# Kernel optimization log

Measured on AMD Instinct MI355X. Metric: run time of the kernel, lower is better.

Reference implementation:

```python
import jax, jax.numpy as jnp
import numpy as np

N = 50000   # nodes
E = 800000  # edges
IN, H, OUT = 64, 512, 128


def _lin_init(key, out_dim, in_dim):
    kw, kb = jax.random.split(key)
    bound = 1.0 / np.sqrt(in_dim)
    W = jax.random.uniform(kw, (out_dim, in_dim), jnp.float32, -bound, bound)
    b = jax.random.uniform(kb, (out_dim,), jnp.float32, -bound, bound)
    return W, b


def setup_inputs() -> dict:
    key = jax.random.key(0)
    ks = jax.random.split(key, 10)
    x = jax.random.normal(ks[0], (N, IN), jnp.float32)
    edge_index = jax.random.randint(ks[1], (2, E), 0, N, jnp.int64)
    W_s1, b_s1 = _lin_init(ks[2], H, IN)
    W_s2, b_s2 = _lin_init(ks[3], H, H)
    W_s3, b_s3 = _lin_init(ks[4], H, H)
    W_s4, b_s4 = _lin_init(ks[5], H, H)
    W_m1, b_m1 = _lin_init(ks[6], OUT, H)
    W_m2, b_m2 = _lin_init(ks[7], OUT, OUT)
    W_l1, b_l1 = _lin_init(ks[8], OUT, H)
    W_l2, b_l2 = _lin_init(ks[9], OUT, OUT)
    return {"x": x, "edge_index": edge_index,
            "W_s1": W_s1, "b_s1": b_s1, "W_s2": W_s2, "b_s2": b_s2,
            "W_s3": W_s3, "b_s3": b_s3, "W_s4": W_s4, "b_s4": b_s4,
            "W_m1": W_m1, "b_m1": b_m1, "W_m2": W_m2, "b_m2": b_m2,
            "W_l1": W_l1, "b_l1": b_l1, "W_l2": W_l2, "b_l2": b_l2}


def _aggregate(h, src, dst):
    # GINConv with default eps=0: (1+eps)*x + sum_{j in N(i)} x_j
    return h + jax.ops.segment_sum(h[src], dst, num_segments=N)


def reference(x, edge_index,
              W_s1, b_s1, W_s2, b_s2, W_s3, b_s3, W_s4, b_s4,
              W_m1, b_m1, W_m2, b_m2, W_l1, b_l1, W_l2, b_l2):
    src, dst = edge_index[0], edge_index[1]
    lrelu = lambda v: jax.nn.leaky_relu(v, 0.1)

    def mlp_shared(h):
        h = lrelu(h @ W_s1.T + b_s1)
        h = lrelu(h @ W_s2.T + b_s2)
        h = lrelu(h @ W_s3.T + b_s3)
        return h @ W_s4.T + b_s4

    def mlp_mu(h):
        return jax.nn.relu(h @ W_m1.T + b_m1) @ W_m2.T + b_m2

    def mlp_logvar(h):
        return jax.nn.relu(h @ W_l1.T + b_l1) @ W_l2.T + b_l2

    h = jax.nn.relu(mlp_shared(_aggregate(x, src, dst)))
    mu = mlp_mu(_aggregate(h, src, dst))
    logvar = mlp_logvar(_aggregate(h, src, dst))
    return (mu, logvar)
```

## Files before the change

### kernel.cpp

```cpp
#include <hip/hip_runtime.h>
#include <hip/hip_bf16.h>
#include <stdint.h>

#define N_NODES 50000
#define N_PAD   50048
#define E_EDGES 800000
#define MT      391

typedef __bf16 bf16x8 __attribute__((ext_vector_type(8)));
typedef __bf16 bf16x4 __attribute__((ext_vector_type(4)));
typedef float  f32x4  __attribute__((ext_vector_type(4)));

#define SCAN_B 1024
__global__ void scan_block(const int* __restrict__ cnt, int* __restrict__ ptr,
                           int* __restrict__ bsum, int n) {
    __shared__ int buf[SCAN_B];
    int i = blockIdx.x * SCAN_B + threadIdx.x;
    int v = (i < n) ? cnt[i] : 0;
    buf[threadIdx.x] = v;
    __syncthreads();
    #pragma unroll
    for (int off = 1; off < SCAN_B; off <<= 1) {
        int t = (threadIdx.x >= (unsigned)off) ? buf[threadIdx.x - off] : 0;
        __syncthreads();
        buf[threadIdx.x] += t;
        __syncthreads();
    }
    if (i < n) ptr[i] = buf[threadIdx.x] - v;
    if (threadIdx.x == SCAN_B - 1) bsum[blockIdx.x] = buf[SCAN_B - 1];
}

__global__ void scan_bsums(const int* __restrict__ bsum, int* __restrict__ boff,
                           int nb, int* __restrict__ total_out) {
    __shared__ int buf[SCAN_B];
    int v = ((int)threadIdx.x < nb) ? bsum[threadIdx.x] : 0;
    buf[threadIdx.x] = v;
    __syncthreads();
    #pragma unroll
    for (int off = 1; off < SCAN_B; off <<= 1) {
        int t = (threadIdx.x >= (unsigned)off) ? buf[threadIdx.x - off] : 0;
        __syncthreads();
        buf[threadIdx.x] += t;
        __syncthreads();
    }
    if ((int)threadIdx.x < nb) boff[threadIdx.x] = buf[threadIdx.x] - v;
    if (threadIdx.x == SCAN_B - 1) *total_out = buf[SCAN_B - 1];
}

__global__ void scan_add(int* __restrict__ ptr, const int* __restrict__ boff, int n) {
    int i = blockIdx.x * SCAN_B + threadIdx.x;
    if (i < n) ptr[i] += boff[blockIdx.x];
}

__global__ void fill_csr(const int* __restrict__ ei, const int* __restrict__ ptr,
                         int* __restrict__ cursor, int* __restrict__ col) {
    int e = blockIdx.x * blockDim.x + threadIdx.x;
    if (e < E_EDGES) {
        int dst = ei[E_EDGES + e];
        int pos = ptr[dst] + atomicAdd(&cursor[dst], 1);
        col[pos] = ei[e];
    }
}

#define XN      3200000
#define WTOT    983040
__global__ void cvt_count(const float* __restrict__ x,
                          const float* __restrict__ Ws1, const float* __restrict__ Ws2,
                          const float* __restrict__ Ws3, const float* __restrict__ Ws4,
                          const float* __restrict__ Wm1, const float* __restrict__ Wl1,
                          const float* __restrict__ Wm2, const float* __restrict__ Wl2,
                          const int* __restrict__ ei,
                          __bf16* __restrict__ xb, __bf16* __restrict__ wbuf,
                          int* __restrict__ cnt) {
    int i = blockIdx.x * blockDim.x + threadIdx.x;
    if (i < XN) { xb[i] = (__bf16)x[i]; return; }
    int j = i - XN;
    if (j < WTOT) {
        const float* s; int o;
        if      (j <  32768) { s = Ws1; o = j; }
        else if (j < 294912) { s = Ws2; o = j -  32768; }
        else if (j < 557056) { s = Ws3; o = j - 294912; }
        else if (j < 819200) { s = Ws4; o = j - 557056; }
        else if (j < 884736) { s = Wm1; o = j - 819200; }
        else if (j < 950272) { s = Wl1; o = j - 884736; }
        else if (j < 966656) { s = Wm2; o = j - 950272; }
        else                 { s = Wl2; o = j - 966656; }
        wbuf[j] = (__bf16)s[o];
        return;
    }
    int e = j - WTOT;
    if (e < E_EDGES) atomicAdd(&cnt[ei[E_EDGES + e]], 1);
}

__global__ __launch_bounds__(256) void agg0_gather(
    const __bf16* __restrict__ xb, const int* __restrict__ ptr,
    const int* __restrict__ col, __bf16* __restrict__ out) {
    int node = blockIdx.x * 4 + (threadIdx.x >> 6);
    int lane = threadIdx.x & 63;
    int g    = lane >> 3;
    int f0   = (lane & 7) << 3;
    if (node >= N_PAD) return;
    long o = (long)node * 64 + f0;
    if (node >= N_NODES) {
        if (g == 0) {
            bf16x8 z;
            #pragma unroll
            for (int i = 0; i < 8; ++i) z[i] = (__bf16)0.0f;
            *(bf16x8*)&out[o] = z;
        }
        return;
    }
    float a[8];
    #pragma unroll
    for (int i = 0; i < 8; ++i) a[i] = 0.0f;
    if (g == 0) {
        bf16x8 s = *(const bf16x8*)&xb[o];
        #pragma unroll
        for (int i = 0; i < 8; ++i) a[i] = (float)s[i];
    }
    int e0 = ptr[node], e1 = ptr[node + 1];
    int e = e0;
    for (; e + 16 <= e1; e += 16) {
        int c0 = col[e + g];
        int c1 = col[e + 8 + g];
        bf16x8 v0 = *(const bf16x8*)&xb[(c0 << 6) + f0];
        bf16x8 v1 = *(const bf16x8*)&xb[(c1 << 6) + f0];
        #pragma unroll
        for (int i = 0; i < 8; ++i) a[i] += (float)v0[i] + (float)v1[i];
    }
    int rem = e1 - e;
    if (rem > 0) {
        int u0 = (g < rem) ? g : 0;        float m0 = (g < rem) ? 1.0f : 0.0f;
        int i1 = g + 8;
        int u1 = (i1 < rem) ? i1 : 0;      float m1 = (i1 < rem) ? 1.0f : 0.0f;
        int c0 = col[e + u0];
        int c1 = col[e + u1];
        bf16x8 v0 = *(const bf16x8*)&xb[(c0 << 6) + f0];
        bf16x8 v1 = *(const bf16x8*)&xb[(c1 << 6) + f0];
        #pragma unroll
        for (int i = 0; i < 8; ++i) a[i] += m0 * (float)v0[i] + m1 * (float)v1[i];
    }
    #pragma unroll
    for (int i = 0; i < 8; ++i) {
        a[i] += __shfl_xor(a[i], 8, 64);
        a[i] += __shfl_xor(a[i], 16, 64);
        a[i] += __shfl_xor(a[i], 32, 64);
    }
    if (g == 0) {
        bf16x8 r;
        #pragma unroll
        for (int i = 0; i < 8; ++i) r[i] = (__bf16)a[i];
        *(bf16x8*)&out[o] = r;
    }
}

__global__ __launch_bounds__(256) void aggt_gather(
    const __bf16* __restrict__ t, const int* __restrict__ ptr,
    const int* __restrict__ col, const float* __restrict__ b_m1,
    const float* __restrict__ b_l1, __bf16* __restrict__ p) {
    int node = blockIdx.x * 8 + (threadIdx.x >> 5);
    if (node >= N_NODES) return;
    int hl = threadIdx.x & 31;
    int f0 = hl << 3;
    float a[8];
    {
        bf16x8 s = *(const bf16x8*)&t[((long)node << 8) + f0];
        #pragma unroll
        for (int i = 0; i < 8; ++i) a[i] = (float)s[i];
    }
    int e0 = ptr[node], e1 = ptr[node + 1];
    int e = e0;
    for (; e + 8 <= e1; e += 8) {
        int c[8];
        #pragma unroll
        for (int u = 0; u < 8; ++u) c[u] = col[e + u];
        bf16x8 v[8];
        #pragma unroll
        for (int u = 0; u < 8; ++u) v[u] = *(const bf16x8*)&t[((long)c[u] << 8) + f0];
        #pragma unroll
        for (int u = 0; u < 8; ++u)
            #pragma unroll
            for (int i = 0; i < 8; ++i) a[i] += (float)v[u][i];
    }
    int rem = e1 - e;
    if (rem > 0) {
        #pragma unroll
        for (int u = 0; u < 7; ++u) {
            int   uu = (u < rem) ? u : 0;
            float m  = (u < rem) ? 1.0f : 0.0f;
            int   cc = col[e + uu];
            bf16x8 v = *(const bf16x8*)&t[((long)cc << 8) + f0];
            #pragma unroll
            for (int i = 0; i < 8; ++i) a[i] += m * (float)v[i];
        }
    }
    const float* bp = (f0 < 128) ? (b_m1 + f0) : (b_l1 + (f0 - 128));
    f32x4 b0 = *(const f32x4*)bp;
    f32x4 b1 = *(const f32x4*)(bp + 4);
    bf16x8 r;
    #pragma unroll
    for (int i = 0; i < 4; ++i) r[i]     = (__bf16)fmaxf(a[i]     + b0[i], 0.0f);
    #pragma unroll
    for (int i = 0; i < 4; ++i) r[4 + i] = (__bf16)fmaxf(a[4 + i] + b1[i], 0.0f);
    *(bf16x8*)&p[((long)node << 8) + f0] = r;
}

__device__ __forceinline__ void gl_lds16(const __bf16* g, __bf16* l) {
    __builtin_amdgcn_global_load_lds(
        (const __attribute__((address_space(1))) uint32_t*)g,
        (__attribute__((address_space(3))) uint32_t*)l, 16, 0, 0);
}

#define P_WAITN(n) asm volatile("s_waitcnt vmcnt(" #n ")" ::: "memory")
#define P_WAIT0    asm volatile("s_waitcnt vmcnt(0)" ::: "memory")
#define P_LGKM0    asm volatile("s_waitcnt lgkmcnt(0)" ::: "memory")
#define P_BAR      __builtin_amdgcn_s_barrier()
#define P_SGB      __builtin_amdgcn_sched_barrier(0)
#define SLOTE      2048

__device__ __forceinline__ void stage_w64(const __bf16* __restrict__ W, int Kdim,
                                          int k0, int wn,
                                          __bf16* __restrict__ slot, int lane) {
    int r16 = lane >> 2, sl = lane & 3;
    #pragma unroll
    for (int i = 0; i < 4; ++i) {
        int rl = i * 16 + r16;
        int kt = sl ^ ((rl >> 1) & 3);
        gl_lds16(W + (long)(wn + rl) * Kdim + k0 + kt * 8, slot + i * 512);
    }
}

__device__ __forceinline__ void stage_wp32(const __bf16* __restrict__ W, int k0,
                                           int wnp, __bf16* __restrict__ slot,
                                           int lane) {
    int r8 = lane >> 3, sl = lane & 7;
    #pragma unroll
    for (int i = 0; i < 4; ++i) {
        int rl = i * 8 + r8;
        int kt = sl ^ (rl & 7);
        gl_lds16(W + (long)(wnp + rl) * 512 + k0 + kt * 8, slot + i * 512);
    }
}

__device__ __forceinline__ void chunk_mfma4L(const __bf16* __restrict__ sAct,
    const __bf16* __restrict__ buf, int c, int rA, int q,
    f32x4 (&acc)[4][4]) {
    const int g   = c * 4 + q;
    const int sla = ((g & 56) | ((g & 7) ^ (rA & 7))) << 3;
    bf16x8 af[4], bfr[4];
    #pragma unroll
    for (int mi = 0; mi < 4; ++mi)
        af[mi] = *(const bf16x8*)&sAct[(mi * 16 + rA) * 512 + sla];
    #pragma unroll
    for (int ni = 0; ni < 4; ++ni) {
        int wrl = ni * 16 + rA;
        bfr[ni] = *(const bf16x8*)&buf[wrl * 32 + ((q ^ ((wrl >> 1) & 3)) << 3)];
    }
    #pragma unroll
    for (int mi = 0; mi < 4; ++mi)
        #pragma unroll
        for (int ni = 0; ni < 4; ++ni)
            acc[mi][ni] = __builtin_amdgcn_mfma_f32_16x16x32_bf16(
                af[mi], bfr[ni], acc[mi][ni], 0, 0, 0);
}

__device__ __forceinline__ void chunk_mfma_a0L(const __bf16* __restrict__ act0,
    const __bf16* __restrict__ buf, int c, int rA, int q,
    f32x4 (&acc)[4][4]) {
    const int g   = c * 4 + q;
    const int sla = (g ^ (rA & 7)) << 3;
    bf16x8 af[4], bfr[4];
    #pragma unroll
    for (int mi = 0; mi < 4; ++mi)
        af[mi] = *(const bf16x8*)&act0[(mi * 16 + rA) * 64 + sla];
    #pragma unroll
    for (int ni = 0; ni < 4; ++ni) {
        int wrl = ni * 16 + rA;
        bfr[ni] = *(const bf16x8*)&buf[wrl * 32 + ((q ^ ((wrl >> 1) & 3)) << 3)];
    }
    #pragma unroll
    for (int mi = 0; mi < 4; ++mi)
        #pragma unroll
        for (int ni = 0; ni < 4; ++ni)
            acc[mi][ni] = __builtin_amdgcn_mfma_f32_16x16x32_bf16(
                af[mi], bfr[ni], acc[mi][ni], 0, 0, 0);
}

__device__ __forceinline__ void chunk_mfma_projL(const __bf16* __restrict__ sAct,
    const __bf16* __restrict__ buf, int c, int rA, int q,
    f32x4 (&accp)[4][2]) {
    #pragma unroll
    for (int s = 0; s < 2; ++s) {
        const int g   = c * 8 + s * 4 + q;
        const int sla = ((g & 56) | ((g & 7) ^ (rA & 7))) << 3;
        bf16x8 af[4], bfr[2];
        #pragma unroll
        for (int mi = 0; mi < 4; ++mi)
            af[mi] = *(const bf16x8*)&sAct[(mi * 16 + rA) * 512 + sla];
        #pragma unroll
        for (int ni = 0; ni < 2; ++ni) {
            int wrl = ni * 16 + rA;
            int gB  = s * 4 + q;
            bfr[ni] = *(const bf16x8*)&buf[wrl * 64 + ((gB ^ (wrl & 7)) << 3)];
        }
        #pragma unroll
        for (int mi = 0; mi < 4; ++mi)
            #pragma unroll
            for (int ni = 0; ni < 2; ++ni)
                accp[mi][ni] = __builtin_amdgcn_mfma_f32_16x16x32_bf16(
                    af[mi], bfr[ni], accp[mi][ni], 0, 0, 0);
    }
}

template <int ACTn>
__device__ __forceinline__ void writeback_act(__bf16* __restrict__ sAct,
    f32x4 (&acc)[4][4], const float* __restrict__ bv,
    int wn, int ccol, int crow) {
    #pragma unroll
    for (int mi = 0; mi < 4; ++mi)
        #pragma unroll
        for (int ni = 0; ni < 4; ++ni) {
            int cc = wn + ni * 16 + ccol;
            int g  = cc >> 3;
            #pragma unroll
            for (int p = 0; p < 4; ++p) {
                int rr = mi * 16 + crow + p;
                float v = acc[mi][ni][p] + bv[ni];
                if (ACTn == 1) v = (v > 0.0f) ? v : 0.1f * v;
                else           v = fmaxf(v, 0.0f);
                int sl = (g & 56) | ((g & 7) ^ (rr & 7));
                sAct[rr * 512 + sl * 8 + (cc & 7)] = (__bf16)v;
            }
        }
}

template <int ACTn, bool NPROJ>
__device__ __forceinline__ void layer512_wv(
    __bf16* __restrict__ sAct, __bf16* __restrict__ sA, __bf16* __restrict__ sB,
    const __bf16* __restrict__ W, const __bf16* __restrict__ Wn,
    const float* __restrict__ bv,
    int wn, int wnp, int rA, int q, int ccol, int crow, int lane) {
    f32x4 acc[4][4];
    #pragma unroll
    for (int i = 0; i < 4; ++i)
        #pragma unroll
        for (int j = 0; j < 4; ++j) acc[i][j] = (f32x4)0.0f;
    #pragma unroll
    for (int c = 0; c < 16; ++c) {
        P_WAITN(4);
        __bf16* cur = (c & 1) ? sB : sA;
        chunk_mfma4L(sAct, cur, c, rA, q, acc);
        P_SGB;
        if (c <= 13)      stage_w64(W, 512, (c + 2) * 32, wn, cur, lane);
        else if (!NPROJ)  stage_w64(Wn, 512, (c - 14) * 32, wn, cur, lane);
        else              stage_wp32(Wn, (c - 14) * 64, wnp, cur, lane);
    }
    P_BAR;
    writeback_act<ACTn>(sAct, acc, bv, wn, ccol, crow);
    P_LGKM0; P_BAR;
}

__global__ __launch_bounds__(512) void mlp_fused(
    const __bf16* __restrict__ a0,
    const __bf16* __restrict__ w1, const float* __restrict__ b1,
    const __bf16* __restrict__ w2, const float* __restrict__ b2,
    const __bf16* __restrict__ w3, const float* __restrict__ b3,
    const __bf16* __restrict__ w4, const float* __restrict__ b4,
    const __bf16* __restrict__ wp,
    __bf16* __restrict__ tg)
{
    __shared__ __bf16 lds[69632];
    __bf16* act0  = lds;
    __bf16* sAct  = lds + 4096;
    __bf16* slots = lds + 36864;

    const int tid  = threadIdx.x;
    const int wid  = tid >> 6;
    const int lane = tid & 63;
    const long blockRow = (long)blockIdx.x * 64;

    const int rA   = lane & 15;
    const int q    = lane >> 4;
    const int ccol = lane & 15;
    const int crow = (lane >> 4) << 2;
    const int wn   = wid << 6;
    const int wnp  = wid << 5;

    __bf16* sA = slots + (wid * 2) * SLOTE;
    __bf16* sB = sA + SLOTE;

    {
        int srow = lane >> 3;
        int skg  = (lane & 7) ^ srow;
        gl_lds16(a0 + (blockRow + wid * 8 + srow) * 64 + skg * 8, act0 + wid * 512);
    }
    stage_w64(w1, 64, 0,  wn, sA, lane);
    stage_w64(w1, 64, 32, wn, sB, lane);
    float bv1[4], bv2[4], bv3[4], bv4[4];
    #pragma unroll
    for (int ni = 0; ni < 4; ++ni) {
        int idx = wn + ni * 16 + ccol;
        bv1[ni] = b1[idx]; bv2[ni] = b2[idx]; bv3[ni] = b3[idx]; bv4[ni] = b4[idx];
    }

    asm volatile("s_waitcnt vmcnt(0) lgkmcnt(0)" ::: "memory");
    P_BAR;

    {
        f32x4 acc[4][4];
        #pragma unroll
        for (int i = 0; i < 4; ++i)
            #pragma unroll
            for (int j = 0; j < 4; ++j) acc[i][j] = (f32x4)0.0f;
        chunk_mfma_a0L(act0, sA, 0, rA, q, acc);
        P_SGB;
        stage_w64(w2, 512, 0, wn, sA, lane);
        P_WAITN(4);
        chunk_mfma_a0L(act0, sB, 1, rA, q, acc);
        P_SGB;
        stage_w64(w2, 512, 32, wn, sB, lane);
        P_BAR;
        writeback_act<1>(sAct, acc, bv1, wn, ccol, crow);
        P_LGKM0; P_BAR;
    }

    layer512_wv<1, false>(sAct, sA, sB, w2, w3, bv2, wn, wnp, rA, q, ccol, crow, lane);
    layer512_wv<1, false>(sAct, sA, sB, w3, w4, bv3, wn, wnp, rA, q, ccol, crow, lane);
    layer512_wv<2, true >(sAct, sA, sB, w4, wp, bv4, wn, wnp, rA, q, ccol, crow, lane);

    {
        f32x4 accp[4][2];
        #pragma unroll
        for (int i = 0; i < 4; ++i)
            #pragma unroll
            for (int j = 0; j < 2; ++j) accp[i][j] = (f32x4)0.0f;
        #pragma unroll
        for (int c = 0; c < 8; ++c) {
            if (c == 7) { P_WAIT0; } else { P_WAITN(4); }
            __bf16* cur = (c & 1) ? sB : sA;
            chunk_mfma_projL(sAct, cur, c, rA, q, accp);
            P_SGB;
            if (c <= 5) stage_wp32(wp, (c + 2) * 64, wnp, cur, lane);
        }
        P_BAR;
        __bf16* s0 = slots;
        #pragma unroll
        for (int mi = 0; mi < 4; ++mi)
            #pragma unroll
            for (int ni = 0; ni < 2; ++ni)
                #pragma unroll
                for (int p = 0; p < 4; ++p)
                    s0[(mi * 16 + crow + p) * 256 + wnp + ni * 16 + ccol] =
                        (__bf16)accp[mi][ni][p];
        __syncthreads();
        int rr = tid >> 3;
        int c0 = (tid & 7) << 5;
        const bf16x8* s = (const bf16x8*)&s0[rr * 256 + c0];
        __bf16* d = tg + (blockRow + rr) * 256 + c0;
        #pragma unroll
        for (int i = 0; i < 4; ++i) *(bf16x8*)(d + i * 8) = s[i];
    }
}

template <int NCOL>
__device__ __forceinline__ void swizzle_xy(int bid, int& x, int& y) {
    int grp  = bid / (8 * NCOL);
    int rem  = bid - grp * (8 * NCOL);
    int base = grp * 8;
    int width = MT - base; if (width > 8) width = 8;
    x = base + rem % width;
    y = rem / width;
}

template <int ACT, bool BIAS, bool OUT_BF16, bool MCHK>
__device__ __forceinline__ void gemm_core(
    const __bf16* __restrict__ A, int lda, const __bf16* __restrict__ W,
    const float* __restrict__ bias, void* __restrict__ Cout, int ldc,
    int K, long Mstore, long blockRow, int blockCol,
    __bf16* __restrict__ smem) {
    __bf16* As = smem;
    __bf16* Ws = smem + 8192;
    const int tid  = threadIdx.x;
    const int wid  = tid >> 6;
    const int lane = tid & 63;
    const int wm = (wid >> 1) << 6;
    const int wn = (wid & 1) << 6;

    f32x4 acc[4][4];
    #pragma unroll
    for (int i = 0; i < 4; ++i)
        #pragma unroll
        for (int j = 0; j < 4; ++j) acc[i][j] = (f32x4)0.0f;

    const int srow = lane >> 3;
    const int skg  = (lane & 7) ^ srow;
    const __bf16* gA[4]; const __bf16* gW[4];
    __bf16 *lA[4], *lW[4];
    #pragma unroll
    for (int i = 0; i < 4; ++i) {
        int c = wid * 4 + i;
        gA[i] = A + (blockRow + c * 8 + srow) * (long)lda + skg * 8;
        gW[i] = W + ((long)blockCol + c * 8 + srow) * (long)K + skg * 8;
        lA[i] = As + c * 512;
        lW[i] = Ws + c * 512;
    }

    const int rA = lane & 15;
    const int q  = lane >> 4;
    const int r7 = rA & 7;

    for (int k0 = 0; k0 < K; k0 += 64) {
        #pragma unroll
        for (int i = 0; i < 4; ++i) gl_lds16(gA[i] + k0, lA[i]);
        #pragma unroll
        for (int i = 0; i < 4; ++i) gl_lds16(gW[i] + k0, lW[i]);
        __syncthreads();

        #pragma unroll
        for (int s = 0; s < 2; ++s) {
            const int slot = ((s * 4 + q) ^ r7) * 8;
            bf16x8 af[4], bf[4];
            #pragma unroll
            for (int mi = 0; mi < 4; ++mi)
                af[mi] = *(const bf16x8*)&As[(wm + mi * 16 + rA) * 64 + slot];
            #pragma unroll
            for (int ni = 0; ni < 4; ++ni)
                bf[ni] = *(const bf16x8*)&Ws[(wn + ni * 16 + rA) * 64 + slot];
            #pragma unroll
            for (int mi = 0; mi < 4; ++mi)
                #pragma unroll
                for (int ni = 0; ni < 4; ++ni)
                    acc[mi][ni] = __builtin_amdgcn_mfma_f32_16x16x32_bf16(
                        af[mi], bf[ni], acc[mi][ni], 0, 0, 0);
        }
        __syncthreads();
    }

    const int ccol = lane & 15;
    const int crow = (lane >> 4) << 2;
    if (OUT_BF16 && !MCHK) {
        #pragma unroll
        for (int mi = 0; mi < 4; ++mi) {
            #pragma unroll
            for (int ni = 0; ni < 4; ++ni) {
                int gc = wn + ni * 16 + ccol;
                float bv = BIAS ? bias[blockCol + gc] : 0.0f;
                #pragma unroll
                for (int r = 0; r < 4; ++r) {
                    float v = acc[mi][ni][r] + bv;
                    if (ACT == 1) v = (v > 0.0f) ? v : 0.1f * v;
                    else if (ACT == 2) v = fmaxf(v, 0.0f);
                    smem[(wm + mi * 16 + crow + r) * 128 + gc] = (__bf16)v;
                }
            }
        }
        __syncthreads();
        #pragma unroll
        for (int i = 0; i < 8; ++i) {
            int o   = (i * 256 + tid) * 8;
            int row = o >> 7;
            int co  = o & 127;
            *(bf16x8*)((__bf16*)Cout + (blockRow + row) * (long)ldc + blockCol + co) =
                *(const bf16x8*)&smem[o];
        }
    } else if (!OUT_BF16) {
        float* fsmem = (float*)smem;
        #pragma unroll
        for (int half = 0; half < 2; ++half) {
            __syncthreads();
            if ((wm >> 6) == half) {
                #pragma unroll
                for (int mi = 0; mi < 4; ++mi) {
                    #pragma unroll
                    for (int ni = 0; ni < 4; ++ni) {
                        int gc = wn + ni * 16 + ccol;
                        float bv = BIAS ? bias[blockCol + gc] : 0.0f;
                        #pragma unroll
                        for (int r = 0; r < 4; ++r) {
                            float v = acc[mi][ni][r] + bv;
                            if (ACT == 1) v = (v > 0.0f) ? v : 0.1f * v;
                            else if (ACT == 2) v = fmaxf(v, 0.0f);
                            fsmem[(mi * 16 + crow + r) * 128 + gc] = v;
                        }
                    }
                }
            }
            __syncthreads();
            #pragma unroll
            for (int i = 0; i < 8; ++i) {
                int o   = i * 256 + tid;
                int row = o >> 5;
                int co  = (o & 31) * 4;
                long gr = blockRow + half * 64 + row;
                if (!MCHK || gr < Mstore)
                    *(f32x4*)((float*)Cout + gr * (long)ldc + blockCol + co) =
                        *(const f32x4*)&fsmem[o * 4];
            }
        }
    } else {
        #pragma unroll
        for (int mi = 0; mi < 4; ++mi) {
            #pragma unroll
            for (int ni = 0; ni < 4; ++ni) {
                long gr0 = blockRow + wm + mi * 16 + crow;
                int  gc  = blockCol + wn + ni * 16 + ccol;
                float bv = BIAS ? bias[gc] : 0.0f;
                #pragma unroll
                for (int r = 0; r < 4; ++r) {
                    long gr = gr0 + r;
                    if (!MCHK || gr < Mstore) {
                        float v = acc[mi][ni][r] + bv;
                        if (ACT == 1) v = (v > 0.0f) ? v : 0.1f * v;
                        else if (ACT == 2) v = fmaxf(v, 0.0f);
                        ((__bf16*)Cout)[gr * ldc + gc] = (__bf16)v;
                    }
                }
            }
        }
    }
}

__global__ __launch_bounds__(256) void gemm_heads(
    const __bf16* __restrict__ p, const __bf16* __restrict__ wm2,
    const float* __restrict__ b_m2, float* __restrict__ mu,
    const __bf16* __restrict__ wl2, const float* __restrict__ b_l2,
    float* __restrict__ lv) {
    __shared__ __bf16 smem[128 * 128];
    int x, hd;
    swizzle_xy<2>(blockIdx.x, x, hd);
    if (hd == 0)
        gemm_core<0, true, false, true>(p, 256, wm2, b_m2, mu, 128, 128, N_NODES,
                                        (long)x * 128, 0, smem);
    else
        gemm_core<0, true, false, true>(p + 128, 256, wl2, b_l2, lv, 128, 128, N_NODES,
                                        (long)x * 128, 0, smem);
}

extern "C" void kernel_launch(void* const* d_in, const int* in_sizes, int n_in,
                              void* d_out, int out_size, void* d_ws, size_t ws_size,
                              hipStream_t stream) {
    const float* x    = (const float*)d_in[0];
    const int*   ei   = (const int*)d_in[1];
    const float* W_s1 = (const float*)d_in[2];
    const float* b_s1 = (const float*)d_in[3];
    const float* W_s2 = (const float*)d_in[4];
    const float* b_s2 = (const float*)d_in[5];
    const float* W_s3 = (const float*)d_in[6];
    const float* b_s3 = (const float*)d_in[7];
    const float* W_s4 = (const float*)d_in[8];
    const float* b_s4 = (const float*)d_in[9];
    const float* W_m1 = (const float*)d_in[10];
    const float* b_m1 = (const float*)d_in[11];
    const float* W_m2 = (const float*)d_in[12];
    const float* b_m2 = (const float*)d_in[13];
    const float* W_l1 = (const float*)d_in[14];
    const float* b_l1 = (const float*)d_in[15];
    const float* W_l2 = (const float*)d_in[16];
    const float* b_l2 = (const float*)d_in[17];

    char* ws = (char*)d_ws;
    size_t off = 0;
    auto carve = [&](size_t bytes) -> void* {
        void* p = ws + off;
        off = (off + bytes + 255) & ~(size_t)255;
        return p;
    };
    int* ptr  = (int*)carve((size_t)(N_NODES + 1) * 4);
    int* col  = (int*)carve((size_t)E_EDGES * 4);
    int* bsum = (int*)carve(SCAN_B * 4);
    int* boff = (int*)carve(SCAN_B * 4);
    __bf16* wbuf = (__bf16*)carve((size_t)WTOT * 2);
    __bf16* w1  = wbuf;
    __bf16* w2  = wbuf +  32768;
    __bf16* w3  = wbuf + 294912;
    __bf16* w4  = wbuf + 557056;
    __bf16* wml = wbuf + 819200;
    __bf16* wm2 = wbuf + 950272;
    __bf16* wl2 = wbuf + 966656;
    __bf16* xb    = (__bf16*)carve((size_t)XN * 2);
    __bf16* agg0b = (__bf16*)carve((size_t)N_PAD * 64 * 2);
    __bf16* B1    = (__bf16*)carve((size_t)N_PAD * 512 * 2);
    __bf16* B2    = (__bf16*)carve((size_t)N_PAD * 512 * 2);

    int* cnt = (int*)B1;
    int* cur = (int*)B2;

    (void)hipMemsetAsync(cnt, 0, (size_t)N_NODES * 4, stream);
    (void)hipMemsetAsync(cur, 0, (size_t)N_NODES * 4, stream);

    cvt_count<<<(XN + WTOT + E_EDGES + 255) / 256, 256, 0, stream>>>(
        x, W_s1, W_s2, W_s3, W_s4, W_m1, W_l1, W_m2, W_l2, ei, xb, wbuf, cnt);

    const int NB = (N_NODES + SCAN_B - 1) / SCAN_B;
    scan_block<<<NB, SCAN_B, 0, stream>>>(cnt, ptr, bsum, N_NODES);
    scan_bsums<<<1, SCAN_B, 0, stream>>>(bsum, boff, NB, &ptr[N_NODES]);
    scan_add<<<NB, SCAN_B, 0, stream>>>(ptr, boff, N_NODES);
    fill_csr<<<E_EDGES / 256, 256, 0, stream>>>(ei, ptr, cur, col);

    agg0_gather<<<N_PAD / 4, 256, 0, stream>>>(xb, ptr, col, agg0b);

    __bf16* t = B1;
    mlp_fused<<<N_PAD / 64, 512, 0, stream>>>(agg0b, w1, b_s1, w2, b_s2,
                                              w3, b_s3, w4, b_s4, wml, t);

    __bf16* p = B2;
    aggt_gather<<<(N_NODES + 7) / 8, 256, 0, stream>>>(t, ptr, col, b_m1, b_l1, p);

    float* mu = (float*)d_out;
    float* lv = mu + (size_t)N_NODES * 128;
    gemm_heads<<<MT * 2, 256, 0, stream>>>(p, wm2, b_m2, mu, wl2, b_l2, lv);
}
```

Baseline: 426.0 us.

## Fuse second-layer neighbor gather into the mu/logvar head GEMM kernel

Replaces the separate aggregation kernel (which wrote the aggregated, bias+ReLU hidden tensor p to global memory) and the head GEMM kernel with a single kernel. Each block gathers neighbor sums for its 128 nodes and one head's 128 columns directly into swizzled LDS, then runs the 128x128x128 MFMA GEMM and writes fp32 outputs. This removes the p write/read round-trip and one launch. In exchange each block does its gather with only 256 threads in 8 sequential passes, which may reduce memory-level parallelism, and it uses 64KB of LDS per block, which limits occupancy.

```diff
diff --git a/kernel.cpp b/kernel.cpp
--- a/kernel.cpp
+++ b/kernel.cpp
@@ -154,61 +154,20 @@
     }
 }
 
-__global__ __launch_bounds__(256) void aggt_gather(
-    const __bf16* __restrict__ t, const int* __restrict__ ptr,
-    const int* __restrict__ col, const float* __restrict__ b_m1,
-    const float* __restrict__ b_l1, __bf16* __restrict__ p) {
-    int node = blockIdx.x * 8 + (threadIdx.x >> 5);
-    if (node >= N_NODES) return;
-    int hl = threadIdx.x & 31;
-    int f0 = hl << 3;
-    float a[8];
-    {
-        bf16x8 s = *(const bf16x8*)&t[((long)node << 8) + f0];
-        #pragma unroll
-        for (int i = 0; i < 8; ++i) a[i] = (float)s[i];
-    }
-    int e0 = ptr[node], e1 = ptr[node + 1];
-    int e = e0;
-    for (; e + 8 <= e1; e += 8) {
-        int c[8];
-        #pragma unroll
-        for (int u = 0; u < 8; ++u) c[u] = col[e + u];
-        bf16x8 v[8];
-        #pragma unroll
-        for (int u = 0; u < 8; ++u) v[u] = *(const bf16x8*)&t[((long)c[u] << 8) + f0];
-        #pragma unroll
-        for (int u = 0; u < 8; ++u)
-            #pragma unroll
-            for (int i = 0; i < 8; ++i) a[i] += (float)v[u][i];
-    }
-    int rem = e1 - e;
-    if (rem > 0) {
-        #pragma unroll
-        for (int u = 0; u < 7; ++u) {
-            int   uu = (u < rem) ? u : 0;
-            float m  = (u < rem) ? 1.0f : 0.0f;
-            int   cc = col[e + uu];
-            bf16x8 v = *(const bf16x8*)&t[((long)cc << 8) + f0];
-            #pragma unroll
-            for (int i = 0; i < 8; ++i) a[i] += m * (float)v[i];
-        }
-    }
-    const float* bp = (f0 < 128) ? (b_m1 + f0) : (b_l1 + (f0 - 128));
-    f32x4 b0 = *(const f32x4*)bp;
-    f32x4 b1 = *(const f32x4*)(bp + 4);
-    bf16x8 r;
-    #pragma unroll
-    for (int i = 0; i < 4; ++i) r[i]     = (__bf16)fmaxf(a[i]     + b0[i], 0.0f);
-    #pragma unroll
-    for (int i = 0; i < 4; ++i) r[4 + i] = (__bf16)fmaxf(a[4 + i] + b1[i], 0.0f);
-    *(bf16x8*)&p[((long)node << 8) + f0] = r;
-}
-
 __device__ __forceinline__ void gl_lds16(const __bf16* g, __bf16* l) {
     __builtin_amdgcn_global_load_lds(
         (const __attribute__((address_space(1))) uint32_t*)g,
         (__attribute__((address_space(3))) uint32_t*)l, 16, 0, 0);
+}
+
+template <int NCOL>
+__device__ __forceinline__ void swizzle_xy(int bid, int& x, int& y) {
+    int grp  = bid / (8 * NCOL);
+    int rem  = bid - grp * (8 * NCOL);
+    int base = grp * 8;
+    int width = MT - base; if (width > 8) width = 8;
+    x = base + rem % width;
+    y = rem / width;
 }
 
 #define P_WAITN(n) asm volatile("s_waitcnt vmcnt(" #n ")" ::: "memory")
@@ -462,178 +421,158 @@
     }
 }
 
-template <int NCOL>
-__device__ __forceinline__ void swizzle_xy(int bid, int& x, int& y) {
-    int grp  = bid / (8 * NCOL);
-    int rem  = bid - grp * (8 * NCOL);
-    int base = grp * 8;
-    int width = MT - base; if (width > 8) width = 8;
-    x = base + rem % width;
-    y = rem / width;
-}
-
-template <int ACT, bool BIAS, bool OUT_BF16, bool MCHK>
-__device__ __forceinline__ void gemm_core(
-    const __bf16* __restrict__ A, int lda, const __bf16* __restrict__ W,
-    const float* __restrict__ bias, void* __restrict__ Cout, int ldc,
-    int K, long Mstore, long blockRow, int blockCol,
-    __bf16* __restrict__ smem) {
-    __bf16* As = smem;
-    __bf16* Ws = smem + 8192;
+__global__ __launch_bounds__(256) void heads_fused(
+    const __bf16* __restrict__ t, const int* __restrict__ ptr,
+    const int* __restrict__ col,
+    const float* __restrict__ b_m1, const float* __restrict__ b_l1,
+    const __bf16* __restrict__ wm2, const float* __restrict__ b_m2,
+    float* __restrict__ mu,
+    const __bf16* __restrict__ wl2, const float* __restrict__ b_l2,
+    float* __restrict__ lv)
+{
+    __shared__ __bf16 lds[32768];
+    __bf16* Al = lds;
+    __bf16* Wl = lds + 16384;
+
     const int tid  = threadIdx.x;
     const int wid  = tid >> 6;
     const int lane = tid & 63;
-    const int wm = (wid >> 1) << 6;
-    const int wn = (wid & 1) << 6;
-
-    f32x4 acc[4][4];
-    #pragma unroll
-    for (int i = 0; i < 4; ++i)
-        #pragma unroll
-        for (int j = 0; j < 4; ++j) acc[i][j] = (f32x4)0.0f;
-
-    const int srow = lane >> 3;
-    const int skg  = (lane & 7) ^ srow;
-    const __bf16* gA[4]; const __bf16* gW[4];
-    __bf16 *lA[4], *lW[4];
-    #pragma unroll
-    for (int i = 0; i < 4; ++i) {
-        int c = wid * 4 + i;
-        gA[i] = A + (blockRow + c * 8 + srow) * (long)lda + skg * 8;
-        gW[i] = W + ((long)blockCol + c * 8 + srow) * (long)K + skg * 8;
-        lA[i] = As + c * 512;
-        lW[i] = Ws + c * 512;
-    }
-
-    const int rA = lane & 15;
-    const int q  = lane >> 4;
-    const int r7 = rA & 7;
-
-    for (int k0 = 0; k0 < K; k0 += 64) {
-        #pragma unroll
-        for (int i = 0; i < 4; ++i) gl_lds16(gA[i] + k0, lA[i]);
-        #pragma unroll
-        for (int i = 0; i < 4; ++i) gl_lds16(gW[i] + k0, lW[i]);
-        __syncthreads();
-
-        #pragma unroll
-        for (int s = 0; s < 2; ++s) {
-            const int slot = ((s * 4 + q) ^ r7) * 8;
-            bf16x8 af[4], bf[4];
-            #pragma unroll
-            for (int mi = 0; mi < 4; ++mi)
-                af[mi] = *(const bf16x8*)&As[(wm + mi * 16 + rA) * 64 + slot];
-            #pragma unroll
-            for (int ni = 0; ni < 4; ++ni)
-                bf[ni] = *(const bf16x8*)&Ws[(wn + ni * 16 + rA) * 64 + slot];
-            #pragma unroll
-            for (int mi = 0; mi < 4; ++mi)
+    int x, hd;
+    swizzle_xy<2>(blockIdx.x, x, hd);
+    const long rowBase = (long)x * 128;
+
+    const __bf16* W   = hd ? wl2 : wm2;
+    const float*  bs1 = hd ? b_l1 : b_m1;
+    const float*  bs2 = hd ? b_l2 : b_m2;
+    float*        outp = hd ? lv : mu;
+    const int     tcol = hd << 7;
+
+    {
+        int r4  = lane >> 4;
+        int gsl = lane & 15;
+        #pragma unroll
+        for (int i = 0; i < 8; ++i) {
+            int row = wid * 32 + i * 4 + r4;
+            int g   = (gsl & 8) | ((gsl & 7) ^ (row & 7));
+            gl_lds16(W + (long)row * 128 + g * 8, Wl + (wid * 32 + i * 4) * 128);
+        }
+    }
+
+    const int lane16 = tid & 15;
+    const int ng     = tid >> 4;
+    f32x4 bg0 = *(const f32x4*)&bs1[lane16 * 8];
+    f32x4 bg1 = *(const f32x4*)&bs1[lane16 * 8 + 4];
+
+    for (int pass = 0; pass < 8; ++pass) {
+        int  nl   = pass * 16 + ng;
+        long node = rowBase + nl;
+        bf16x8 r;
+        if (node < N_NODES) {
+            float a[8];
+            bf16x8 s = *(const bf16x8*)&t[node * 256 + tcol + lane16 * 8];
+            #pragma unroll
+            for (int i = 0; i < 8; ++i) a[i] = (float)s[i];
+            int e0 = ptr[node], e1 = ptr[node + 1];
+            int e = e0;
+            for (; e + 8 <= e1; e += 8) {
+                int c[8];
                 #pragma unroll
-                for (int ni = 0; ni < 4; ++ni)
-                    acc[mi][ni] = __builtin_amdgcn_mfma_f32_16x16x32_bf16(
-                        af[mi], bf[ni], acc[mi][ni], 0, 0, 0);
-        }
-        __syncthreads();
-    }
-
+                for (int u = 0; u < 8; ++u) c[u] = col[e + u];
+                bf16x8 v[8];
+                #pragma unroll
+                for (int u = 0; u < 8; ++u)
+                    v[u] = *(const bf16x8*)&t[(long)c[u] * 256 + tcol + lane16 * 8];
+                #pragma unroll
+                for (int u = 0; u < 8; ++u)
+                    #pragma unroll
+                    for (int i = 0; i < 8; ++i) a[i] += (float)v[u][i];
+            }
+            int rem = e1 - e;
+            if (rem > 0) {
+                #pragma unroll
+                for (int u = 0; u < 7; ++u) {
+                    int   uu = (u < rem) ? u : 0;
+                    float m  = (u < rem) ? 1.0f : 0.0f;
+                    int   cc = col[e + uu];
+                    bf16x8 v = *(const bf16x8*)&t[(long)cc * 256 + tcol + lane16 * 8];
+                    #pragma unroll
+                    for (int i = 0; i < 8; ++i) a[i] += m * (float)v[i];
+                }
+            }
+            #pragma unroll
+            for (int i = 0; i < 4; ++i) r[i]     = (__bf16)fmaxf(a[i]     + bg0[i], 0.0f);
+            #pragma unroll
+            for (int i = 0; i < 4; ++i) r[4 + i] = (__bf16)fmaxf(a[4 + i] + bg1[i], 0.0f);
+        } else {
+            #pragma unroll
+            for (int i = 0; i < 8; ++i) r[i] = (__bf16)0.0f;
+        }
+        int sl = (lane16 & 8) | ((lane16 & 7) ^ (nl & 7));
+        *(bf16x8*)&Al[nl * 128 + sl * 8] = r;
+    }
+
+    const int rA   = lane & 15;
+    const int q    = lane >> 4;
     const int ccol = lane & 15;
     const int crow = (lane >> 4) << 2;
-    if (OUT_BF16 && !MCHK) {
+    const int wm   = (wid >> 1) << 6;
+    const int wn   = (wid & 1) << 6;
+    float bv2[4];
+    #pragma unroll
+    for (int ni = 0; ni < 4; ++ni) bv2[ni] = bs2[wn + ni * 16 + ccol];
+
+    asm volatile("s_waitcnt vmcnt(0) lgkmcnt(0)" ::: "memory");
+    __syncthreads();
+
+    f32x4 acc[4][4];
+    #pragma unroll
+    for (int i = 0; i < 4; ++i)
+        #pragma unroll
+        for (int j = 0; j < 4; ++j) acc[i][j] = (f32x4)0.0f;
+    #pragma unroll
+    for (int c = 0; c < 4; ++c) {
+        const int g = c * 4 + q;
+        bf16x8 af[4], bf[4];
         #pragma unroll
         for (int mi = 0; mi < 4; ++mi) {
-            #pragma unroll
-            for (int ni = 0; ni < 4; ++ni) {
-                int gc = wn + ni * 16 + ccol;
-                float bv = BIAS ? bias[blockCol + gc] : 0.0f;
-                #pragma unroll
-                for (int r = 0; r < 4; ++r) {
-                    float v = acc[mi][ni][r] + bv;
-                    if (ACT == 1) v = (v > 0.0f) ? v : 0.1f * v;
-                    else if (ACT == 2) v = fmaxf(v, 0.0f);
-                    smem[(wm + mi * 16 + crow + r) * 128 + gc] = (__bf16)v;
-                }
-            }
-        }
-        __syncthreads();
-        #pragma unroll
-        for (int i = 0; i < 8; ++i) {
-            int o   = (i * 256 + tid) * 8;
-            int row = o >> 7;
-            int co  = o & 127;
-            *(bf16x8*)((__bf16*)Cout + (blockRow + row) * (long)ldc + blockCol + co) =
-                *(const bf16x8*)&smem[o];
-        }
-    } else if (!OUT_BF16) {
-        float* fsmem = (float*)smem;
-        #pragma unroll
-        for (int half = 0; half < 2; ++half) {
-            __syncthreads();
-            if ((wm >> 6) == half) {
-                #pragma unroll
-                for (int mi = 0; mi < 4; ++mi) {
-                    #pragma unroll
-                    for (int ni = 0; ni < 4; ++ni) {
-                        int gc = wn + ni * 16 + ccol;
-                        float bv = BIAS ? bias[blockCol + gc] : 0.0f;
-                        #pragma unroll
-                        for (int r = 0; r < 4; ++r) {
-                            float v = acc[mi][ni][r] + bv;
-                            if (ACT == 1) v = (v > 0.0f) ? v : 0.1f * v;
-                            else if (ACT == 2) v = fmaxf(v, 0.0f);
-                            fsmem[(mi * 16 + crow + r) * 128 + gc] = v;
-                        }
-                    }
-                }
-            }
-            __syncthreads();
-            #pragma unroll
-            for (int i = 0; i < 8; ++i) {
-                int o   = i * 256 + tid;
-                int row = o >> 5;
-                int co  = (o & 31) * 4;
-                long gr = blockRow + half * 64 + row;
-                if (!MCHK || gr < Mstore)
-                    *(f32x4*)((float*)Cout + gr * (long)ldc + blockCol + co) =
-                        *(const f32x4*)&fsmem[o * 4];
-            }
-        }
-    } else {
-        #pragma unroll
-        for (int mi = 0; mi < 4; ++mi) {
-            #pragma unroll
-            for (int ni = 0; ni < 4; ++ni) {
-                long gr0 = blockRow + wm + mi * 16 + crow;
-                int  gc  = blockCol + wn + ni * 16 + ccol;
-                float bv = BIAS ? bias[gc] : 0.0f;
-                #pragma unroll
-                for (int r = 0; r < 4; ++r) {
-                    long gr = gr0 + r;
-                    if (!MCHK || gr < Mstore) {
-                        float v = acc[mi][ni][r] + bv;
-                        if (ACT == 1) v = (v > 0.0f) ? v : 0.1f * v;
-                        else if (ACT == 2) v = fmaxf(v, 0.0f);
-                        ((__bf16*)Cout)[gr * ldc + gc] = (__bf16)v;
-                    }
-                }
-            }
-        }
-    }
-}
-
-__global__ __launch_bounds__(256) void gemm_heads(
-    const __bf16* __restrict__ p, const __bf16* __restrict__ wm2,
-    const float* __restrict__ b_m2, float* __restrict__ mu,
-    const __bf16* __restrict__ wl2, const float* __restrict__ b_l2,
-    float* __restrict__ lv) {
-    __shared__ __bf16 smem[128 * 128];
-    int x, hd;
-    swizzle_xy<2>(blockIdx.x, x, hd);
-    if (hd == 0)
-        gemm_core<0, true, false, true>(p, 256, wm2, b_m2, mu, 128, 128, N_NODES,
-                                        (long)x * 128, 0, smem);
-    else
-        gemm_core<0, true, false, true>(p + 128, 256, wl2, b_l2, lv, 128, 128, N_NODES,
-                                        (long)x * 128, 0, smem);
+            int r  = wm + mi * 16 + rA;
+            int sl = (g & 8) | ((g & 7) ^ (r & 7));
+            af[mi] = *(const bf16x8*)&Al[r * 128 + sl * 8];
+        }
+        #pragma unroll
+        for (int ni = 0; ni < 4; ++ni) {
+            int r  = wn + ni * 16 + rA;
+            int sl = (g & 8) | ((g & 7) ^ (r & 7));
+            bf[ni] = *(const bf16x8*)&Wl[r * 128 + sl * 8];
+        }
+        #pragma unroll
+        for (int mi = 0; mi < 4; ++mi)
+            #pragma unroll
+            for (int ni = 0; ni < 4; ++ni)
+                acc[mi][ni] = __builtin_amdgcn_mfma_f32_16x16x32_bf16(
+                    af[mi], bf[ni], acc[mi][ni], 0, 0, 0);
+    }
+
+    __syncthreads();
+    float* fs = (float*)lds;
+    #pragma unroll
+    for (int mi = 0; mi < 4; ++mi)
+        #pragma unroll
+        for (int ni = 0; ni < 4; ++ni)
+            #pragma unroll
+            for (int p = 0; p < 4; ++p)
+                fs[(wm + mi * 16 + crow + p) * 128 + wn + ni * 16 + ccol] =
+                    acc[mi][ni][p] + bv2[ni];
+    __syncthreads();
+    #pragma unroll
+    for (int i = 0; i < 16; ++i) {
+        int idx = i * 256 + tid;
+        int row = idx >> 5;
+        int c0  = (idx & 31) * 4;
+        long gr = rowBase + row;
+        if (gr < N_NODES)
+            *(f32x4*)&outp[gr * 128 + c0] = *(const f32x4*)&fs[idx * 4];
+    }
 }
 
 extern "C" void kernel_launch(void* const* d_in, const int* in_sizes, int n_in,
@@ -703,10 +642,8 @@
     mlp_fused<<<N_PAD / 64, 512, 0, stream>>>(agg0b, w1, b_s1, w2, b_s2,
                                               w3, b_s3, w4, b_s4, wml, t);
 
-    __bf16* p = B2;
-    aggt_gather<<<(N_NODES + 7) / 8, 256, 0, stream>>>(t, ptr, col, b_m1, b_l1, p);
-
     float* mu = (float*)d_out;
     float* lv = mu + (size_t)N_NODES * 128;
-    gemm_heads<<<MT * 2, 256, 0, stream>>>(p, wm2, b_m2, mu, wl2, b_l2, lv);
-}
+    heads_fused<<<MT * 2, 256, 0, stream>>>(t, ptr, col, b_m1, b_l1,
+                                            wm2, b_m2, mu, wl2, b_l2, lv);
+}
```

After: 438.7 us. 3.0% more time.
